# Kernel tuning notes

Hardware: AMD Instinct MI355X
Metric: run time of the kernel (lower is better)

Reference implementation:

```python
import jax, jax.numpy as jnp
import numpy as np

N_DRUG = 50000
N_DIS = 50000
D = 128      # input feature dim (lazily inferred by GCNConv(-1, h))
H = 128      # hidden_channels
OUT = 64     # out_channels
E = 800000   # edges per relation
L = 2        # num_layers
NUM_REL = 4  # [drug-drug, dis-dis, drug->dis, dis->drug]


def setup_inputs() -> dict:
    key = jax.random.key(0)
    ks = jax.random.split(key, 10)
    x_drug = jax.random.normal(ks[0], (N_DRUG, D), jnp.float32)
    x_dis = jax.random.normal(ks[1], (N_DIS, D), jnp.float32)
    ei_dd = jax.random.randint(ks[2], (2, E), 0, N_DRUG, dtype=jnp.int32)
    ei_ss = jax.random.randint(ks[3], (2, E), 0, N_DIS, dtype=jnp.int32)
    ei_ds = jax.random.randint(ks[4], (2, E), 0, N_DRUG, dtype=jnp.int32)  # row<N_DRUG, col<N_DIS (equal sizes)
    ei_sd = jax.random.randint(ks[5], (2, E), 0, N_DIS, dtype=jnp.int32)
    # per-layer, per-relation GCN weights (glorot-ish scale) and biases
    Ws = jax.random.normal(ks[6], (L, NUM_REL, D, H), jnp.float32) * (1.0 / np.sqrt(D))
    bs = jnp.zeros((L, NUM_REL, H), jnp.float32)
    lin_w = jax.random.normal(ks[7], (OUT, H), jnp.float32) * (1.0 / np.sqrt(H))
    lin_b = jnp.zeros((OUT,), jnp.float32)
    return {"x_drug": x_drug, "x_dis": x_dis, "ei_dd": ei_dd, "ei_ss": ei_ss,
            "ei_ds": ei_ds, "ei_sd": ei_sd, "Ws": Ws, "bs": bs,
            "lin_w": lin_w, "lin_b": lin_b}


def _gcn(x_src, ei, n_src, n_dst, W, b, self_loops):
    """GCNConv: symmetric degree-normalized gather -> scatter-add -> linear."""
    row, col = ei[0], ei[1]
    if self_loops:  # homogeneous relation: add self loops (n_src == n_dst)
        idx = jnp.arange(n_dst, dtype=row.dtype)
        row = jnp.concatenate([row, idx])
        col = jnp.concatenate([col, idx])
    ones = jnp.ones(row.shape[0], x_src.dtype)
    deg_s = jax.ops.segment_sum(ones, row, num_segments=n_src)
    deg_d = jax.ops.segment_sum(ones, col, num_segments=n_dst)
    dinv_s = jnp.where(deg_s > 0, jax.lax.rsqrt(jnp.maximum(deg_s, 1.0)), 0.0)
    dinv_d = jnp.where(deg_d > 0, jax.lax.rsqrt(jnp.maximum(deg_d, 1.0)), 0.0)
    norm = dinv_s[row] * dinv_d[col]                      # [E]
    h = x_src @ W                                         # [n_src, H]
    out = jax.ops.segment_sum(h[row] * norm[:, None], col, num_segments=n_dst)
    return out + b


def reference(x_drug, x_dis, ei_dd, ei_ss, ei_ds, ei_sd, Ws, bs, lin_w, lin_b):
    for l in range(L):
        drug_new = (_gcn(x_drug, ei_dd, N_DRUG, N_DRUG, Ws[l, 0], bs[l, 0], True)
                    + _gcn(x_dis, ei_sd, N_DIS, N_DRUG, Ws[l, 3], bs[l, 3], False))
        dis_new = (_gcn(x_dis, ei_ss, N_DIS, N_DIS, Ws[l, 1], bs[l, 1], True)
                   + _gcn(x_drug, ei_ds, N_DRUG, N_DIS, Ws[l, 2], bs[l, 2], False))
        x_drug = jax.nn.relu(drug_new)
        x_dis = jax.nn.relu(dis_new)
    return (x_drug @ lin_w.T + lin_b, x_dis @ lin_w.T + lin_b)
```

## Files before the change

### kernel.cpp

```cpp
#include <hip/hip_runtime.h>

#define NV   50000
#define FD   128
#define NE   800000
#define NOUT 64
#define NBIN 196
#define CH   2048
#define NBLK 391
#define SCAN_L (NBIN * NBLK)
#define SCHUNK 2048
#define NSCH ((SCAN_L + SCHUNK - 1) / SCHUNK)
#define CAP2 12288

typedef unsigned short bf16_t;
typedef unsigned short u16;
typedef unsigned char  u8;
typedef __attribute__((ext_vector_type(8))) short bf16x8;
typedef __attribute__((ext_vector_type(4))) float f32x4;

__device__ __forceinline__ bf16_t f2bf(float f) {
  unsigned u = __builtin_bit_cast(unsigned, f);
  return (bf16_t)((u + 0x7fffu + ((u >> 16) & 1u)) >> 16);
}
__device__ __forceinline__ float bflo(unsigned v) { return __builtin_bit_cast(float, v << 16); }
__device__ __forceinline__ float bfhi(unsigned v) { return __builtin_bit_cast(float, v & 0xffff0000u); }

struct Ptr4 { const int* p[4]; };


__global__ __launch_bounds__(256) void p0_hist(Ptr4 rows, Ptr4 cols,
                                               int* __restrict__ blockCnt) {
  const int r = blockIdx.y, blk = blockIdx.x, t = threadIdx.x;
  __shared__ int cd[NBIN], cs[NBIN];
  for (int i = t; i < NBIN; i += 256) { cd[i] = 0; cs[i] = 0; }
  __syncthreads();
  const int e0 = blk * CH;
  const int n = min(CH, NE - e0);
  const int* rw = rows.p[r] + e0;
  const int* cl = cols.p[r] + e0;
  for (int i = t; i < n; i += 256) {
    atomicAdd(&cd[cl[i] >> 8], 1);
    atomicAdd(&cs[rw[i] >> 8], 1);
  }
  __syncthreads();
  int* bd = blockCnt + (size_t)(r * 2 + 0) * SCAN_L;
  int* bs = blockCnt + (size_t)(r * 2 + 1) * SCAN_L;
  for (int i = t; i < NBIN; i += 256) {
    bd[i * NBLK + blk] = cd[i];
    bs[i * NBLK + blk] = cs[i];
  }
}

__global__ __launch_bounds__(256) void scan_pass1(const int* __restrict__ blockCnt,
                                                  int* __restrict__ chunkSum) {
  const int r2 = blockIdx.y, chunk = blockIdx.x, t = threadIdx.x;
  const int* a = blockCnt + (size_t)r2 * SCAN_L + chunk * SCHUNK;
  const int n = min(SCHUNK, SCAN_L - chunk * SCHUNK);
  int s = 0;
  for (int i = t; i < n; i += 256) s += a[i];
  __shared__ int sm[256];
  sm[t] = s;
  __syncthreads();
  #pragma unroll
  for (int off = 128; off > 0; off >>= 1) {
    if (t < off) sm[t] += sm[t + off];
    __syncthreads();
  }
  if (t == 0) chunkSum[r2 * NSCH + chunk] = sm[0];
}

__global__ __launch_bounds__(512) void scan_pass2(int* __restrict__ chunkSum,
                                                  int* __restrict__ bucketBase) {
  const int t = threadIdx.x;
  __shared__ int sm[8 * NSCH];
  if (t < 8 * NSCH) sm[t] = chunkSum[t];
  __syncthreads();
  if (t < 8) {
    int run = 0;
    for (int j = 0; j < NSCH; ++j) {
      int v = sm[t * NSCH + j];
      sm[t * NSCH + j] = run;
      run += v;
    }
    bucketBase[t * (NBIN + 1) + NBIN] = NE;
  }
  __syncthreads();
  if (t < 8 * NSCH) chunkSum[t] = sm[t];
}

__global__ __launch_bounds__(256) void scan_pass3(int* __restrict__ blockCnt,
                                                  const int* __restrict__ chunkSum,
                                                  int* __restrict__ bucketBase) {
  const int r2 = blockIdx.y, chunk = blockIdx.x, t = threadIdx.x;
  int* a = blockCnt + (size_t)r2 * SCAN_L + chunk * SCHUNK;
  const int gbase = chunk * SCHUNK;
  const int n = min(SCHUNK, SCAN_L - gbase);
  const int idx0 = t * 8;
  int v[8];
  int s = 0;
  #pragma unroll
  for (int j = 0; j < 8; ++j) {
    int id = idx0 + j;
    v[j] = (id < n) ? a[id] : 0;
    s += v[j];
  }
  __shared__ int sm[256];
  sm[t] = s;
  __syncthreads();
  for (int off = 1; off < 256; off <<= 1) {
    int x = (t >= off) ? sm[t - off] : 0;
    __syncthreads();
    sm[t] += x;
    __syncthreads();
  }
  int pre = ((t == 0) ? 0 : sm[t - 1]) + chunkSum[r2 * NSCH + chunk];
  #pragma unroll
  for (int j = 0; j < 8; ++j) {
    int id = idx0 + j;
    if (id < n) {
      int val = v[j];
      a[id] = pre;
      int g = gbase + id;
      if (g % NBLK == 0) bucketBase[r2 * (NBIN + 1) + g / NBLK] = pre;
      pre += val;
    }
  }
}

__global__ __launch_bounds__(256) void p1_scatter(Ptr4 rows, Ptr4 cols,
                                                  const int* __restrict__ blockCnt,
                                                  unsigned* __restrict__ pairD,
                                                  u8* __restrict__ srcb) {
  const int r = blockIdx.y, blk = blockIdx.x, t = threadIdx.x;
  const int e0 = blk * CH;
  const int n = min(CH, NE - e0);
  const int* rw = rows.p[r] + e0;
  const int* cl = cols.p[r] + e0;

  __shared__ int cnt[256], sc[256], lofs[256], cnt2[256], baseT[256];
  __shared__ unsigned pr[CH];
  __shared__ u8 binb[CH];
  __shared__ u8 pay8[CH];

  cnt[t] = 0; cnt2[t] = 0;
  __syncthreads();
  for (int i = t; i < n; i += 256) atomicAdd(&cnt[cl[i] >> 8], 1);
  __syncthreads();
  sc[t] = cnt[t];
  __syncthreads();
  for (int off = 1; off < 256; off <<= 1) {
    int v = (t >= off) ? sc[t - off] : 0;
    __syncthreads();
    sc[t] += v;
    __syncthreads();
  }
  lofs[t] = (t == 0) ? 0 : sc[t - 1];
  if (t < NBIN) baseT[t] = blockCnt[(size_t)(r * 2 + 0) * SCAN_L + t * NBLK + blk];
  __syncthreads();
  for (int i = t; i < n; i += 256) {
    int c = cl[i];
    int bin = c >> 8;
    int rank = atomicAdd(&cnt2[bin], 1);
    int p = lofs[bin] + rank;
    pr[p] = ((unsigned)(c & 255) << 16) | (unsigned)rw[i];
    binb[p] = (u8)bin;
  }
  __syncthreads();
  {
    unsigned* pd = pairD + (size_t)r * NE;
    for (int i = t; i < n; i += 256) {
      int bin = binb[i];
      pd[baseT[bin] + (i - lofs[bin])] = pr[i];
    }
  }
  __syncthreads();

  cnt[t] = 0; cnt2[t] = 0;
  __syncthreads();
  for (int i = t; i < n; i += 256) atomicAdd(&cnt[rw[i] >> 8], 1);
  __syncthreads();
  sc[t] = cnt[t];
  __syncthreads();
  for (int off = 1; off < 256; off <<= 1) {
    int v = (t >= off) ? sc[t - off] : 0;
    __syncthreads();
    sc[t] += v;
    __syncthreads();
  }
  lofs[t] = (t == 0) ? 0 : sc[t - 1];
  if (t < NBIN) baseT[t] = blockCnt[(size_t)(r * 2 + 1) * SCAN_L + t * NBLK + blk];
  __syncthreads();
  for (int i = t; i < n; i += 256) {
    int sv = rw[i];
    int bin = sv >> 8;
    int rank = atomicAdd(&cnt2[bin], 1);
    int p = lofs[bin] + rank;
    pay8[p] = (u8)(sv & 255);
    binb[p] = (u8)bin;
  }
  __syncthreads();
  {
    u8* sb = srcb + (size_t)r * NE;
    for (int i = t; i < n; i += 256) {
      int bin = binb[i];
      sb[baseT[bin] + (i - lofs[bin])] = pay8[i];
    }
  }
}

__global__ __launch_bounds__(256) void p2_csr(const unsigned* __restrict__ pairD,
                                              const int* __restrict__ bucketBase,
                                              u16* __restrict__ srcidx,
                                              int* __restrict__ rowptr,
                                              float* __restrict__ dinvD) {
  const int r = blockIdx.y, bin = blockIdx.x, t = threadIdx.x;
  const int* bb = bucketBase + (r * 2 + 0) * (NBIN + 1);
  const int base = bb[bin], next = bb[bin + 1];
  const int span = next - base;
  const unsigned* pd = pairD + (size_t)r * NE + base;

  __shared__ int cnt[256], sc[256], ex[256], cnt2[256];
  __shared__ u16 lsrc[CAP2];
  cnt[t] = 0; cnt2[t] = 0;
  __syncthreads();
  for (int i = t; i < span; i += 256) atomicAdd(&cnt[pd[i] >> 16], 1);
  __syncthreads();
  sc[t] = cnt[t];
  __syncthreads();
  for (int off = 1; off < 256; off <<= 1) {
    int v = (t >= off) ? sc[t - off] : 0;
    __syncthreads();
    sc[t] += v;
    __syncthreads();
  }
  ex[t] = (t == 0) ? 0 : sc[t - 1];
  __syncthreads();

  const int node = (bin << 8) + t;
  if (node < NV) {
    rowptr[r * (NV + 1) + node] = base + ex[t];
    float deg = (float)cnt[t];
    dinvD[r * NV + node] = (r < 2) ? rsqrtf(deg + 1.f)
                                   : (deg > 0.f ? rsqrtf(deg) : 0.f);
  }
  if (bin == NBIN - 1 && t == 0) rowptr[r * (NV + 1) + NV] = NE;

  u16* so = srcidx + (size_t)r * NE + base;
  if (span <= CAP2) {
    for (int i = t; i < span; i += 256) {
      unsigned v = pd[i];
      int dl = v >> 16;
      int rank = atomicAdd(&cnt2[dl], 1);
      lsrc[ex[dl] + rank] = (u16)(v & 0xFFFFu);
    }
    __syncthreads();
    for (int i = t; i < span; i += 256) so[i] = lsrc[i];
  } else {
    for (int i = t; i < span; i += 256) {
      unsigned v = pd[i];
      int dl = v >> 16;
      int rank = atomicAdd(&cnt2[dl], 1);
      so[ex[dl] + rank] = (u16)(v & 0xFFFFu);
    }
  }
}

__global__ __launch_bounds__(256) void p2_srcdeg(const u8* __restrict__ srcb,
                                                 const int* __restrict__ bucketBase,
                                                 float* __restrict__ dinvS) {
  const int r = blockIdx.y, bin = blockIdx.x, t = threadIdx.x;
  const int* bb = bucketBase + (r * 2 + 1) * (NBIN + 1);
  const int base = bb[bin], next = bb[bin + 1];
  const int span = next - base;
  const u8* sb = srcb + (size_t)r * NE + base;
  __shared__ int cnt[256];
  cnt[t] = 0;
  __syncthreads();
  for (int i = t; i < span; i += 256) atomicAdd(&cnt[sb[i]], 1);
  __syncthreads();
  int node = (bin << 8) + t;
  if (node < NV) {
    float deg = (float)cnt[t];
    dinvS[r * NV + node] = (r < 2) ? rsqrtf(deg + 1.f)
                                   : (deg > 0.f ? rsqrtf(deg) : 0.f);
  }
}


__global__ __launch_bounds__(256) void xcvt(const float* __restrict__ x,
                                            bf16_t* __restrict__ xb, int n4) {
  int i = blockIdx.x * 256 + threadIdx.x;
  if (i < n4) {
    float4 v = *(const float4*)(x + (size_t)i * 4);
    unsigned a = (unsigned)f2bf(v.x) | ((unsigned)f2bf(v.y) << 16);
    unsigned b = (unsigned)f2bf(v.z) | ((unsigned)f2bf(v.w) << 16);
    *(uint2*)(xb + (size_t)i * 4) = make_uint2(a, b);
  }
}

__global__ __launch_bounds__(256) void wprep(const float* __restrict__ Wsrc,
                                             bf16_t* __restrict__ Wt) {
  int idx = blockIdx.x * 256 + threadIdx.x;
  if (idx < 8 * 128 * 128) {
    int i = idx >> 14, n = (idx >> 7) & 127, k = idx & 127;
    Wt[idx] = f2bf(Wsrc[(size_t)i * 16384 + k * 128 + n]);
  }
}

__global__ __launch_bounds__(256) void gemm_mfma(
    const bf16_t* __restrict__ Xb0, const bf16_t* __restrict__ Wt0,
    const float* __restrict__ dS0, bf16_t* __restrict__ H0,
    const bf16_t* __restrict__ Xb1, const bf16_t* __restrict__ Wt1,
    const float* __restrict__ dS1, bf16_t* __restrict__ H1) {
  const bf16_t* Xb; const bf16_t* Wt; const float* dS; bf16_t* H;
  if (blockIdx.y == 0) { Xb = Xb0; Wt = Wt0; dS = dS0; H = H0; }
  else                 { Xb = Xb1; Wt = Wt1; dS = dS1; H = H1; }

  __shared__ bf16_t Xs[128][136];
  __shared__ bf16_t Wsh[128][136];
  __shared__ float sdS[128];
  const int t = threadIdx.x;
  const int row0 = blockIdx.x * 128;

  #pragma unroll
  for (int j = 0; j < 8; ++j) {
    int r = (t >> 4) + j * 16;
    int c = (t & 15) * 8;
    int gr = row0 + r;
    uint4 v = make_uint4(0u, 0u, 0u, 0u);
    if (gr < NV) v = *(const uint4*)(Xb + (size_t)gr * FD + c);
    *(uint4*)&Xs[r][c] = v;
    *(uint4*)&Wsh[r][c] = *(const uint4*)(Wt + (size_t)r * FD + c);
  }
  if (t < 128) {
    int g = row0 + t;
    sdS[t] = (g < NV) ? dS[g] : 0.f;
  }
  __syncthreads();

  const int wave = t >> 6, lane = t & 63;
  const int lr = lane & 15;
  const int lk = (lane >> 4) * 8;
  const int mb = wave * 32;

  f32x4 acc[2][8];
  #pragma unroll
  for (int m = 0; m < 2; ++m)
    #pragma unroll
    for (int n = 0; n < 8; ++n) acc[m][n] = (f32x4){0.f, 0.f, 0.f, 0.f};

  #pragma unroll
  for (int kc = 0; kc < 128; kc += 32) {
    bf16x8 a0 = *(const bf16x8*)&Xs[mb + lr][kc + lk];
    bf16x8 a1 = *(const bf16x8*)&Xs[mb + 16 + lr][kc + lk];
    bf16x8 b[8];
    #pragma unroll
    for (int n = 0; n < 8; ++n) b[n] = *(const bf16x8*)&Wsh[n * 16 + lr][kc + lk];
    #pragma unroll
    for (int n = 0; n < 8; ++n) {
      acc[0][n] = __builtin_amdgcn_mfma_f32_16x16x32_bf16(a0, b[n], acc[0][n], 0, 0, 0);
      acc[1][n] = __builtin_amdgcn_mfma_f32_16x16x32_bf16(a1, b[n], acc[1][n], 0, 0, 0);
    }
  }

  __syncthreads();
  const int rgrp = (lane >> 4) * 4;
  #pragma unroll
  for (int m = 0; m < 2; ++m)
    #pragma unroll
    for (int n = 0; n < 8; ++n)
      #pragma unroll
      for (int j = 0; j < 4; ++j) {
        int rr = mb + m * 16 + rgrp + j;
        Wsh[rr][n * 16 + lr] = f2bf(acc[m][n][j] * sdS[rr]);
      }
  __syncthreads();

  #pragma unroll
  for (int j = 0; j < 8; ++j) {
    int r = (t >> 4) + j * 16;
    int c = (t & 15) * 8;
    int gr = row0 + r;
    if (gr < NV) *(uint4*)(H + (size_t)gr * FD + c) = *(const uint4*)&Wsh[r][c];
  }
}

__device__ __forceinline__ void gather_acc(const bf16_t* __restrict__ h,
                                           const u16* __restrict__ src,
                                           int p0, int p1, int d,
                                           float& ax, float& ay) {
  int p = p0;
  for (; p + 4 <= p1; p += 4) {
    int s0 = src[p], s1 = src[p + 1], s2 = src[p + 2], s3 = src[p + 3];
    unsigned v0 = *(const unsigned*)(h + ((size_t)s0 << 7) + d);
    unsigned v1 = *(const unsigned*)(h + ((size_t)s1 << 7) + d);
    unsigned v2 = *(const unsigned*)(h + ((size_t)s2 << 7) + d);
    unsigned v3 = *(const unsigned*)(h + ((size_t)s3 << 7) + d);
    ax += bflo(v0); ay += bfhi(v0);
    ax += bflo(v1); ay += bfhi(v1);
    ax += bflo(v2); ay += bfhi(v2);
    ax += bflo(v3); ay += bfhi(v3);
  }
  for (; p < p1; ++p) {
    int s = src[p];
    unsigned v = *(const unsigned*)(h + ((size_t)s << 7) + d);
    ax += bflo(v); ay += bfhi(v);
  }
}

__global__ __launch_bounds__(256) void pull2(
    const bf16_t* __restrict__ hA, const int* __restrict__ rpA, const u16* __restrict__ srcA,
    const float* __restrict__ dDA,
    const bf16_t* __restrict__ hB, const int* __restrict__ rpB, const u16* __restrict__ srcB,
    const float* __restrict__ dDB,
    const float* __restrict__ bA, const float* __restrict__ bB,
    bf16_t* __restrict__ Y) {
  const int i = (blockIdx.x * 256 + threadIdx.x) >> 6;
  const int lane = threadIdx.x & 63;
  if (i >= NV) return;
  const int d = lane * 2;

  float ax, ay;
  {
    unsigned v = *(const unsigned*)(hA + ((size_t)i << 7) + d);
    ax = bflo(v); ay = bfhi(v);
  }
  gather_acc(hA, srcA, rpA[i], rpA[i + 1], d, ax, ay);
  float bx = 0.f, by = 0.f;
  gather_acc(hB, srcB, rpB[i], rpB[i + 1], d, bx, by);

  float wA = dDA[i], wB = dDB[i];
  float ox = fmaf(ax, wA, fmaf(bx, wB, bA[d] + bB[d]));
  float oy = fmaf(ay, wA, fmaf(by, wB, bA[d + 1] + bB[d + 1]));
  unsigned pk = (unsigned)f2bf(fmaxf(ox, 0.f)) | ((unsigned)f2bf(fmaxf(oy, 0.f)) << 16);
  *(unsigned*)(Y + (size_t)i * FD + d) = pk;
}

__global__ __launch_bounds__(256) void linear64(const bf16_t* __restrict__ Xb,
                                                const float* __restrict__ lw,
                                                const float* __restrict__ lb,
                                                float* __restrict__ Out) {
  __shared__ float Wt[128][68];
  __shared__ float Xs[64][132];
  const int tid = threadIdx.x;
  const int row0 = blockIdx.x * 64;

  for (int i = tid * 4; i < 64 * 128; i += 1024) {
    float4 v = *(const float4*)(lw + i);
    int o = i >> 7, h = i & 127;
    Wt[h + 0][o] = v.x; Wt[h + 1][o] = v.y; Wt[h + 2][o] = v.z; Wt[h + 3][o] = v.w;
  }
  for (int i = tid * 8; i < 64 * 128; i += 2048) {
    int rr = i >> 7, cc = i & 127;
    int gr = row0 + rr;
    uint4 v = make_uint4(0u, 0u, 0u, 0u);
    if (gr < NV) v = *(const uint4*)(Xb + (size_t)gr * FD + cc);
    unsigned* pv = (unsigned*)&v;
    #pragma unroll
    for (int q = 0; q < 4; ++q) {
      Xs[rr][cc + q * 2]     = bflo(pv[q]);
      Xs[rr][cc + q * 2 + 1] = bfhi(pv[q]);
    }
  }
  __syncthreads();

  const int tx = tid & 15, ty = tid >> 4;
  float acc[4][4];
  #pragma unroll
  for (int i = 0; i < 4; ++i)
    #pragma unroll
    for (int j = 0; j < 4; ++j) acc[i][j] = 0.f;

  for (int k = 0; k < 128; k += 4) {
    float4 xr[4], w[4];
    #pragma unroll
    for (int i = 0; i < 4; ++i) xr[i] = *(const float4*)&Xs[ty * 4 + i][k];
    #pragma unroll
    for (int j = 0; j < 4; ++j) w[j] = *(const float4*)&Wt[k + j][tx * 4];
    #pragma unroll
    for (int i = 0; i < 4; ++i) {
      const float* xv = (const float*)&xr[i];
      #pragma unroll
      for (int j = 0; j < 4; ++j) {
        float x = xv[j];
        acc[i][0] = fmaf(x, w[j].x, acc[i][0]);
        acc[i][1] = fmaf(x, w[j].y, acc[i][1]);
        acc[i][2] = fmaf(x, w[j].z, acc[i][2]);
        acc[i][3] = fmaf(x, w[j].w, acc[i][3]);
      }
    }
  }
  float4 bias = *(const float4*)(lb + tx * 4);
  #pragma unroll
  for (int i = 0; i < 4; ++i) {
    int gr = row0 + ty * 4 + i;
    if (gr < NV) {
      *(float4*)(Out + (size_t)gr * NOUT + tx * 4) =
          make_float4(acc[i][0] + bias.x, acc[i][1] + bias.y,
                      acc[i][2] + bias.z, acc[i][3] + bias.w);
    }
  }
}


extern "C" void kernel_launch(void* const* d_in, const int* in_sizes, int n_in,
                              void* d_out, int out_size, void* d_ws, size_t ws_size,
                              hipStream_t stream) {
  const float* x_drug = (const float*)d_in[0];
  const float* x_dis  = (const float*)d_in[1];
  const int* ei[4] = { (const int*)d_in[2], (const int*)d_in[3],
                       (const int*)d_in[4], (const int*)d_in[5] };
  const float* Ws = (const float*)d_in[6];
  const float* bs = (const float*)d_in[7];
  const float* lw = (const float*)d_in[8];
  const float* lb = (const float*)d_in[9];
  float* out = (float*)d_out;

  char* p = (char*)d_ws;
  auto take = [&](size_t bytes) -> void* {
    char* q = p;
    p += (bytes + 255) & ~(size_t)255;
    return (void*)q;
  };
  int* blockCnt   = (int*)take((size_t)8 * SCAN_L * sizeof(int));
  int* chunkSum   = (int*)take((size_t)8 * NSCH * sizeof(int));
  int* bucketBase = (int*)take((size_t)8 * (NBIN + 1) * sizeof(int));
  unsigned* pairD = (unsigned*)take((size_t)4 * NE * sizeof(unsigned));
  u8* srcb        = (u8*)take((size_t)4 * NE);
  u16* srcidx     = (u16*)take((size_t)4 * NE * sizeof(u16));
  int* rowptr     = (int*)take((size_t)4 * (NV + 1) * sizeof(int));
  float* dinvS    = (float*)take((size_t)4 * NV * sizeof(float));
  float* dinvD    = (float*)take((size_t)4 * NV * sizeof(float));
  bf16_t* hA  = (bf16_t*)take((size_t)NV * FD * sizeof(bf16_t));
  bf16_t* hB  = (bf16_t*)take((size_t)NV * FD * sizeof(bf16_t));
  bf16_t* xdb = (bf16_t*)take((size_t)NV * FD * sizeof(bf16_t));
  bf16_t* xsb = (bf16_t*)take((size_t)NV * FD * sizeof(bf16_t));
  bf16_t* Wtb = (bf16_t*)take((size_t)8 * FD * FD * sizeof(bf16_t));
  bf16_t* XD1 = (bf16_t*)take((size_t)NV * FD * sizeof(bf16_t));
  bf16_t* XS1 = (bf16_t*)take((size_t)NV * FD * sizeof(bf16_t));
  bf16_t* XD2 = (bf16_t*)take((size_t)NV * FD * sizeof(bf16_t));
  bf16_t* XS2 = (bf16_t*)take((size_t)NV * FD * sizeof(bf16_t));

  Ptr4 rows = {{ ei[0], ei[1], ei[2], ei[3] }};
  Ptr4 cols = {{ ei[0] + NE, ei[1] + NE, ei[2] + NE, ei[3] + NE }};

  p0_hist<<<dim3(NBLK, 4), 256, 0, stream>>>(rows, cols, blockCnt);
  scan_pass1<<<dim3(NSCH, 8), 256, 0, stream>>>(blockCnt, chunkSum);
  scan_pass2<<<1, 512, 0, stream>>>(chunkSum, bucketBase);
  scan_pass3<<<dim3(NSCH, 8), 256, 0, stream>>>(blockCnt, chunkSum, bucketBase);
  p1_scatter<<<dim3(NBLK, 4), 256, 0, stream>>>(rows, cols, blockCnt, pairD, srcb);
  p2_csr<<<dim3(NBIN, 4), 256, 0, stream>>>(pairD, bucketBase, srcidx, rowptr, dinvD);
  p2_srcdeg<<<dim3(NBIN, 4), 256, 0, stream>>>(srcb, bucketBase, dinvS);
  xcvt<<<(NV * FD / 4 + 255) / 256, 256, 0, stream>>>(x_drug, xdb, NV * FD / 4);
  xcvt<<<(NV * FD / 4 + 255) / 256, 256, 0, stream>>>(x_dis, xsb, NV * FD / 4);
  wprep<<<(8 * FD * FD + 255) / 256, 256, 0, stream>>>(Ws, Wtb);

  const dim3 GEMM_GRID((NV + 127) / 128, 2);
  const int PULL_GRID = NV * 64 / 256;
  const int LIN_GRID = (NV + 63) / 64;
  const bf16_t* xd = xdb;
  const bf16_t* xs = xsb;
  bf16_t* nextd[2] = {XD1, XD2};
  bf16_t* nexts[2] = {XS1, XS2};
  for (int l = 0; l < 2; ++l) {
    const bf16_t* W0 = Wtb + (size_t)(l * 4 + 0) * FD * FD;
    const bf16_t* W1 = Wtb + (size_t)(l * 4 + 1) * FD * FD;
    const bf16_t* W2 = Wtb + (size_t)(l * 4 + 2) * FD * FD;
    const bf16_t* W3 = Wtb + (size_t)(l * 4 + 3) * FD * FD;
    const float* b0 = bs + (l * 4 + 0) * FD;
    const float* b1 = bs + (l * 4 + 1) * FD;
    const float* b2 = bs + (l * 4 + 2) * FD;
    const float* b3 = bs + (l * 4 + 3) * FD;

    gemm_mfma<<<GEMM_GRID, 256, 0, stream>>>(xd, W0, dinvS + 0 * NV, hA,
                                             xs, W3, dinvS + 3 * NV, hB);
    pull2<<<PULL_GRID, 256, 0, stream>>>(
        hA, rowptr + 0 * (NV + 1), srcidx + (size_t)0 * NE, dinvD + 0 * NV,
        hB, rowptr + 3 * (NV + 1), srcidx + (size_t)3 * NE, dinvD + 3 * NV,
        b0, b3, nextd[l]);

    gemm_mfma<<<GEMM_GRID, 256, 0, stream>>>(xs, W1, dinvS + 1 * NV, hA,
                                             xd, W2, dinvS + 2 * NV, hB);
    pull2<<<PULL_GRID, 256, 0, stream>>>(
        hA, rowptr + 1 * (NV + 1), srcidx + (size_t)1 * NE, dinvD + 1 * NV,
        hB, rowptr + 2 * (NV + 1), srcidx + (size_t)2 * NE, dinvD + 2 * NV,
        b1, b2, nexts[l]);

    xd = nextd[l];
    xs = nexts[l];
  }

  linear64<<<LIN_GRID, 256, 0, stream>>>(xd, lw, lb, out);
  linear64<<<LIN_GRID, 256, 0, stream>>>(xs, lw, lb, out + (size_t)NV * NOUT);
}
```

Before: 485.4 us.

## Store GEMM output in feature-sliced layout and pull per slice

Measured after the change: 961.7 us. 1.98x slower.

```diff
diff --git a/kernel.cpp b/kernel.cpp
--- a/kernel.cpp
+++ b/kernel.cpp
@@ -11,6 +11,8 @@
 #define SCHUNK 2048
 #define NSCH ((SCAN_L + SCHUNK - 1) / SCHUNK)
 #define CAP2 12288
+#define NSLICE 8
+#define SDIM 16
 
 typedef unsigned short bf16_t;
 typedef unsigned short u16;
@@ -381,59 +383,69 @@
     int r = (t >> 4) + j * 16;
     int c = (t & 15) * 8;
     int gr = row0 + r;
-    if (gr < NV) *(uint4*)(H + (size_t)gr * FD + c) = *(const uint4*)&Wsh[r][c];
-  }
-}
-
-__device__ __forceinline__ void gather_acc(const bf16_t* __restrict__ h,
-                                           const u16* __restrict__ src,
-                                           int p0, int p1, int d,
-                                           float& ax, float& ay) {
-  int p = p0;
-  for (; p + 4 <= p1; p += 4) {
-    int s0 = src[p], s1 = src[p + 1], s2 = src[p + 2], s3 = src[p + 3];
-    unsigned v0 = *(const unsigned*)(h + ((size_t)s0 << 7) + d);
-    unsigned v1 = *(const unsigned*)(h + ((size_t)s1 << 7) + d);
-    unsigned v2 = *(const unsigned*)(h + ((size_t)s2 << 7) + d);
-    unsigned v3 = *(const unsigned*)(h + ((size_t)s3 << 7) + d);
-    ax += bflo(v0); ay += bfhi(v0);
-    ax += bflo(v1); ay += bfhi(v1);
-    ax += bflo(v2); ay += bfhi(v2);
-    ax += bflo(v3); ay += bfhi(v3);
-  }
-  for (; p < p1; ++p) {
-    int s = src[p];
-    unsigned v = *(const unsigned*)(h + ((size_t)s << 7) + d);
-    ax += bflo(v); ay += bfhi(v);
-  }
-}
-
-__global__ __launch_bounds__(256) void pull2(
+    if (gr < NV) {
+      int slice = c >> 4;
+      int off = c & 15;
+      *(uint4*)(H + ((size_t)slice * NV + gr) * SDIM + off) = *(const uint4*)&Wsh[r][c];
+    }
+  }
+}
+
+__global__ __launch_bounds__(256) void pull_sliced(
     const bf16_t* __restrict__ hA, const int* __restrict__ rpA, const u16* __restrict__ srcA,
     const float* __restrict__ dDA,
     const bf16_t* __restrict__ hB, const int* __restrict__ rpB, const u16* __restrict__ srcB,
     const float* __restrict__ dDB,
     const float* __restrict__ bA, const float* __restrict__ bB,
     bf16_t* __restrict__ Y) {
-  const int i = (blockIdx.x * 256 + threadIdx.x) >> 6;
-  const int lane = threadIdx.x & 63;
+  const int slice = blockIdx.x & 7;
+  const int grp   = blockIdx.x >> 3;
+  const int wave  = threadIdx.x >> 6;
+  const int lane  = threadIdx.x & 63;
+  const int i = grp * 4 + wave;
   if (i >= NV) return;
-  const int d = lane * 2;
-
-  float ax, ay;
+  const int es = lane >> 3, dp = lane & 7;
+
+  const bf16_t* hAs = hA + (size_t)slice * NV * SDIM;
+  const bf16_t* hBs = hB + (size_t)slice * NV * SDIM;
+
+  float ax = 0.f, ay = 0.f;
+  if (es == 0) {
+    unsigned v = *(const unsigned*)(hAs + ((size_t)i << 4) + dp * 2);
+    ax = bflo(v); ay = bfhi(v);
+  }
   {
-    unsigned v = *(const unsigned*)(hA + ((size_t)i << 7) + d);
-    ax = bflo(v); ay = bfhi(v);
-  }
-  gather_acc(hA, srcA, rpA[i], rpA[i + 1], d, ax, ay);
+    int p1 = rpA[i + 1];
+    for (int p = rpA[i] + es; p < p1; p += 8) {
+      int s = srcA[p];
+      unsigned v = *(const unsigned*)(hAs + ((size_t)s << 4) + dp * 2);
+      ax += bflo(v); ay += bfhi(v);
+    }
+  }
   float bx = 0.f, by = 0.f;
-  gather_acc(hB, srcB, rpB[i], rpB[i + 1], d, bx, by);
-
-  float wA = dDA[i], wB = dDB[i];
-  float ox = fmaf(ax, wA, fmaf(bx, wB, bA[d] + bB[d]));
-  float oy = fmaf(ay, wA, fmaf(by, wB, bA[d + 1] + bB[d + 1]));
-  unsigned pk = (unsigned)f2bf(fmaxf(ox, 0.f)) | ((unsigned)f2bf(fmaxf(oy, 0.f)) << 16);
-  *(unsigned*)(Y + (size_t)i * FD + d) = pk;
+  {
+    int p1 = rpB[i + 1];
+    for (int p = rpB[i] + es; p < p1; p += 8) {
+      int s = srcB[p];
+      unsigned v = *(const unsigned*)(hBs + ((size_t)s << 4) + dp * 2);
+      bx += bflo(v); by += bfhi(v);
+    }
+  }
+  #pragma unroll
+  for (int m = 8; m <= 32; m <<= 1) {
+    ax += __shfl_xor(ax, m, 64);
+    ay += __shfl_xor(ay, m, 64);
+    bx += __shfl_xor(bx, m, 64);
+    by += __shfl_xor(by, m, 64);
+  }
+  if (es == 0) {
+    float wA = dDA[i], wB = dDB[i];
+    int d = slice * SDIM + dp * 2;
+    float ox = fmaf(ax, wA, fmaf(bx, wB, bA[d] + bB[d]));
+    float oy = fmaf(ay, wA, fmaf(by, wB, bA[d + 1] + bB[d + 1]));
+    unsigned pk = (unsigned)f2bf(fmaxf(ox, 0.f)) | ((unsigned)f2bf(fmaxf(oy, 0.f)) << 16);
+    *(unsigned*)(Y + (size_t)i * FD + d) = pk;
+  }
 }
 
 __global__ __launch_bounds__(256) void linear64(const bf16_t* __restrict__ Xb,
@@ -556,7 +568,7 @@
   wprep<<<(8 * FD * FD + 255) / 256, 256, 0, stream>>>(Ws, Wtb);
 
   const dim3 GEMM_GRID((NV + 127) / 128, 2);
-  const int PULL_GRID = NV * 64 / 256;
+  const int PULL_GRID = ((NV + 3) / 4) * NSLICE;
   const int LIN_GRID = (NV + 63) / 64;
   const bf16_t* xd = xdb;
   const bf16_t* xs = xsb;
@@ -574,14 +586,14 @@
 
     gemm_mfma<<<GEMM_GRID, 256, 0, stream>>>(xd, W0, dinvS + 0 * NV, hA,
                                              xs, W3, dinvS + 3 * NV, hB);
-    pull2<<<PULL_GRID, 256, 0, stream>>>(
+    pull_sliced<<<PULL_GRID, 256, 0, stream>>>(
         hA, rowptr + 0 * (NV + 1), srcidx + (size_t)0 * NE, dinvD + 0 * NV,
         hB, rowptr + 3 * (NV + 1), srcidx + (size_t)3 * NE, dinvD + 3 * NV,
         b0, b3, nextd[l]);
 
     gemm_mfma<<<GEMM_GRID, 256, 0, stream>>>(xs, W1, dinvS + 1 * NV, hA,
                                              xd, W2, dinvS + 2 * NV, hB);
-    pull2<<<PULL_GRID, 256, 0, stream>>>(
+    pull_sliced<<<PULL_GRID, 256, 0, stream>>>(
         hA, rowptr + 1 * (NV + 1), srcidx + (size_t)1 * NE, dinvD + 1 * NV,
         hB, rowptr + 2 * (NV + 1), srcidx + (size_t)2 * NE, dinvD + 2 * NV,
         b1, b2, nexts[l]);
```

## Batch four relation GEMMs and both pull aggregations per layer into single launches

Applied to the files above, without the earlier changes.

Measured after the change: 422.5 us. -13.0%, faster.

```diff
diff --git a/kernel.cpp b/kernel.cpp
--- a/kernel.cpp
+++ b/kernel.cpp
@@ -13,7 +13,6 @@
 #define CAP2 12288
 
 typedef unsigned short bf16_t;
-typedef unsigned short u16;
 typedef unsigned char  u8;
 typedef __attribute__((ext_vector_type(8))) short bf16x8;
 typedef __attribute__((ext_vector_type(4))) float f32x4;
@@ -210,7 +209,7 @@
 
 __global__ __launch_bounds__(256) void p2_csr(const unsigned* __restrict__ pairD,
                                               const int* __restrict__ bucketBase,
-                                              u16* __restrict__ srcidx,
+                                              int* __restrict__ srcidx,
                                               int* __restrict__ rowptr,
                                               float* __restrict__ dinvD) {
   const int r = blockIdx.y, bin = blockIdx.x, t = threadIdx.x;
@@ -220,7 +219,7 @@
   const unsigned* pd = pairD + (size_t)r * NE + base;
 
   __shared__ int cnt[256], sc[256], ex[256], cnt2[256];
-  __shared__ u16 lsrc[CAP2];
+  __shared__ int lsrc[CAP2];
   cnt[t] = 0; cnt2[t] = 0;
   __syncthreads();
   for (int i = t; i < span; i += 256) atomicAdd(&cnt[pd[i] >> 16], 1);
@@ -245,13 +244,13 @@
   }
   if (bin == NBIN - 1 && t == 0) rowptr[r * (NV + 1) + NV] = NE;
 
-  u16* so = srcidx + (size_t)r * NE + base;
+  int* so = srcidx + (size_t)r * NE + base;
   if (span <= CAP2) {
     for (int i = t; i < span; i += 256) {
       unsigned v = pd[i];
       int dl = v >> 16;
       int rank = atomicAdd(&cnt2[dl], 1);
-      lsrc[ex[dl] + rank] = (u16)(v & 0xFFFFu);
+      lsrc[ex[dl] + rank] = (int)(v & 0xFFFFu);
     }
     __syncthreads();
     for (int i = t; i < span; i += 256) so[i] = lsrc[i];
@@ -260,7 +259,7 @@
       unsigned v = pd[i];
       int dl = v >> 16;
       int rank = atomicAdd(&cnt2[dl], 1);
-      so[ex[dl] + rank] = (u16)(v & 0xFFFFu);
+      so[ex[dl] + rank] = (int)(v & 0xFFFFu);
     }
   }
 }
@@ -307,14 +306,17 @@
   }
 }
 
-__global__ __launch_bounds__(256) void gemm_mfma(
-    const bf16_t* __restrict__ Xb0, const bf16_t* __restrict__ Wt0,
-    const float* __restrict__ dS0, bf16_t* __restrict__ H0,
-    const bf16_t* __restrict__ Xb1, const bf16_t* __restrict__ Wt1,
-    const float* __restrict__ dS1, bf16_t* __restrict__ H1) {
-  const bf16_t* Xb; const bf16_t* Wt; const float* dS; bf16_t* H;
-  if (blockIdx.y == 0) { Xb = Xb0; Wt = Wt0; dS = dS0; H = H0; }
-  else                 { Xb = Xb1; Wt = Wt1; dS = dS1; H = H1; }
+struct G4 {
+  const bf16_t* X[4];
+  const bf16_t* W[4];
+  const float*  dS[4];
+  bf16_t*       H[4];
+};
+
+__global__ __launch_bounds__(256) void gemm_quad(G4 g) {
+  const int q = blockIdx.y;
+  const bf16_t* Xb = g.X[q]; const bf16_t* Wt = g.W[q];
+  const float* dS = g.dS[q]; bf16_t* H = g.H[q];
 
   __shared__ bf16_t Xs[128][136];
   __shared__ bf16_t Wsh[128][136];
@@ -333,8 +335,8 @@
     *(uint4*)&Wsh[r][c] = *(const uint4*)(Wt + (size_t)r * FD + c);
   }
   if (t < 128) {
-    int g = row0 + t;
-    sdS[t] = (g < NV) ? dS[g] : 0.f;
+    int gidx = row0 + t;
+    sdS[t] = (gidx < NV) ? dS[gidx] : 0.f;
   }
   __syncthreads();
 
@@ -385,55 +387,74 @@
   }
 }
 
-__device__ __forceinline__ void gather_acc(const bf16_t* __restrict__ h,
-                                           const u16* __restrict__ src,
-                                           int p0, int p1, int d,
-                                           float& ax, float& ay) {
+__device__ __forceinline__ void gather8(const bf16_t* __restrict__ h,
+                                        const int* __restrict__ src,
+                                        int p0, int p1, int d,
+                                        float& ax, float& ay) {
   int p = p0;
-  for (; p + 4 <= p1; p += 4) {
-    int s0 = src[p], s1 = src[p + 1], s2 = src[p + 2], s3 = src[p + 3];
-    unsigned v0 = *(const unsigned*)(h + ((size_t)s0 << 7) + d);
-    unsigned v1 = *(const unsigned*)(h + ((size_t)s1 << 7) + d);
-    unsigned v2 = *(const unsigned*)(h + ((size_t)s2 << 7) + d);
-    unsigned v3 = *(const unsigned*)(h + ((size_t)s3 << 7) + d);
+  while (p + 8 <= p1) {
+    int s0 = src[p + 0], s1 = src[p + 1], s2 = src[p + 2], s3 = src[p + 3];
+    int s4 = src[p + 4], s5 = src[p + 5], s6 = src[p + 6], s7 = src[p + 7];
+    unsigned v0 = *(const unsigned*)(h + (s0 << 7) + d);
+    unsigned v1 = *(const unsigned*)(h + (s1 << 7) + d);
+    unsigned v2 = *(const unsigned*)(h + (s2 << 7) + d);
+    unsigned v3 = *(const unsigned*)(h + (s3 << 7) + d);
+    unsigned v4 = *(const unsigned*)(h + (s4 << 7) + d);
+    unsigned v5 = *(const unsigned*)(h + (s5 << 7) + d);
+    unsigned v6 = *(const unsigned*)(h + (s6 << 7) + d);
+    unsigned v7 = *(const unsigned*)(h + (s7 << 7) + d);
     ax += bflo(v0); ay += bfhi(v0);
     ax += bflo(v1); ay += bfhi(v1);
     ax += bflo(v2); ay += bfhi(v2);
     ax += bflo(v3); ay += bfhi(v3);
-  }
-  for (; p < p1; ++p) {
+    ax += bflo(v4); ay += bfhi(v4);
+    ax += bflo(v5); ay += bfhi(v5);
+    ax += bflo(v6); ay += bfhi(v6);
+    ax += bflo(v7); ay += bfhi(v7);
+    p += 8;
+  }
+  while (p + 2 <= p1) {
+    int s0 = src[p], s1 = src[p + 1];
+    unsigned v0 = *(const unsigned*)(h + (s0 << 7) + d);
+    unsigned v1 = *(const unsigned*)(h + (s1 << 7) + d);
+    ax += bflo(v0); ay += bfhi(v0);
+    ax += bflo(v1); ay += bfhi(v1);
+    p += 2;
+  }
+  if (p < p1) {
     int s = src[p];
-    unsigned v = *(const unsigned*)(h + ((size_t)s << 7) + d);
+    unsigned v = *(const unsigned*)(h + (s << 7) + d);
     ax += bflo(v); ay += bfhi(v);
   }
 }
 
-__global__ __launch_bounds__(256) void pull2(
-    const bf16_t* __restrict__ hA, const int* __restrict__ rpA, const u16* __restrict__ srcA,
-    const float* __restrict__ dDA,
-    const bf16_t* __restrict__ hB, const int* __restrict__ rpB, const u16* __restrict__ srcB,
-    const float* __restrict__ dDB,
-    const float* __restrict__ bA, const float* __restrict__ bB,
-    bf16_t* __restrict__ Y) {
-  const int i = (blockIdx.x * 256 + threadIdx.x) >> 6;
+struct PullSide {
+  const bf16_t* hA; const int* rpA; const int* srcA; const float* dDA;
+  const bf16_t* hB; const int* rpB; const int* srcB; const float* dDB;
+  const float* bA; const float* bB; bf16_t* Y;
+};
+
+__global__ __launch_bounds__(256) void pull_dual(PullSide s0, PullSide s1) {
+  const PullSide& a = blockIdx.y ? s1 : s0;
+  const int i = __builtin_amdgcn_readfirstlane(blockIdx.x * 4 + (threadIdx.x >> 6));
+  if (i >= NV) return;
   const int lane = threadIdx.x & 63;
-  if (i >= NV) return;
   const int d = lane * 2;
 
   float ax, ay;
   {
-    unsigned v = *(const unsigned*)(hA + ((size_t)i << 7) + d);
+    unsigned v = *(const unsigned*)(a.hA + (i << 7) + d);
     ax = bflo(v); ay = bfhi(v);
   }
-  gather_acc(hA, srcA, rpA[i], rpA[i + 1], d, ax, ay);
+  gather8(a.hA, a.srcA, a.rpA[i], a.rpA[i + 1], d, ax, ay);
   float bx = 0.f, by = 0.f;
-  gather_acc(hB, srcB, rpB[i], rpB[i + 1], d, bx, by);
-
-  float wA = dDA[i], wB = dDB[i];
-  float ox = fmaf(ax, wA, fmaf(bx, wB, bA[d] + bB[d]));
-  float oy = fmaf(ay, wA, fmaf(by, wB, bA[d + 1] + bB[d + 1]));
+  gather8(a.hB, a.srcB, a.rpB[i], a.rpB[i + 1], d, bx, by);
+
+  float wA = a.dDA[i], wB = a.dDB[i];
+  float ox = fmaf(ax, wA, fmaf(bx, wB, a.bA[d] + a.bB[d]));
+  float oy = fmaf(ay, wA, fmaf(by, wB, a.bA[d + 1] + a.bB[d + 1]));
   unsigned pk = (unsigned)f2bf(fmaxf(ox, 0.f)) | ((unsigned)f2bf(fmaxf(oy, 0.f)) << 16);
-  *(unsigned*)(Y + (size_t)i * FD + d) = pk;
+  *(unsigned*)(a.Y + (size_t)i * FD + d) = pk;
 }
 
 __global__ __launch_bounds__(256) void linear64(const bf16_t* __restrict__ Xb,
@@ -527,12 +548,14 @@
   int* bucketBase = (int*)take((size_t)8 * (NBIN + 1) * sizeof(int));
   unsigned* pairD = (unsigned*)take((size_t)4 * NE * sizeof(unsigned));
   u8* srcb        = (u8*)take((size_t)4 * NE);
-  u16* srcidx     = (u16*)take((size_t)4 * NE * sizeof(u16));
+  int* srcidx     = (int*)take((size_t)4 * NE * sizeof(int));
   int* rowptr     = (int*)take((size_t)4 * (NV + 1) * sizeof(int));
   float* dinvS    = (float*)take((size_t)4 * NV * sizeof(float));
   float* dinvD    = (float*)take((size_t)4 * NV * sizeof(float));
   bf16_t* hA  = (bf16_t*)take((size_t)NV * FD * sizeof(bf16_t));
   bf16_t* hB  = (bf16_t*)take((size_t)NV * FD * sizeof(bf16_t));
+  bf16_t* hC  = (bf16_t*)take((size_t)NV * FD * sizeof(bf16_t));
+  bf16_t* hD  = (bf16_t*)take((size_t)NV * FD * sizeof(bf16_t));
   bf16_t* xdb = (bf16_t*)take((size_t)NV * FD * sizeof(bf16_t));
   bf16_t* xsb = (bf16_t*)take((size_t)NV * FD * sizeof(bf16_t));
   bf16_t* Wtb = (bf16_t*)take((size_t)8 * FD * FD * sizeof(bf16_t));
@@ -555,8 +578,8 @@
   xcvt<<<(NV * FD / 4 + 255) / 256, 256, 0, stream>>>(x_dis, xsb, NV * FD / 4);
   wprep<<<(8 * FD * FD + 255) / 256, 256, 0, stream>>>(Ws, Wtb);
 
-  const dim3 GEMM_GRID((NV + 127) / 128, 2);
-  const int PULL_GRID = NV * 64 / 256;
+  const dim3 GEMM_GRID((NV + 127) / 128, 4);
+  const dim3 PULL_GRID((NV + 3) / 4, 2);
   const int LIN_GRID = (NV + 63) / 64;
   const bf16_t* xd = xdb;
   const bf16_t* xs = xsb;
@@ -572,19 +595,26 @@
     const float* b2 = bs + (l * 4 + 2) * FD;
     const float* b3 = bs + (l * 4 + 3) * FD;
 
-    gemm_mfma<<<GEMM_GRID, 256, 0, stream>>>(xd, W0, dinvS + 0 * NV, hA,
-                                             xs, W3, dinvS + 3 * NV, hB);
-    pull2<<<PULL_GRID, 256, 0, stream>>>(
-        hA, rowptr + 0 * (NV + 1), srcidx + (size_t)0 * NE, dinvD + 0 * NV,
-        hB, rowptr + 3 * (NV + 1), srcidx + (size_t)3 * NE, dinvD + 3 * NV,
-        b0, b3, nextd[l]);
-
-    gemm_mfma<<<GEMM_GRID, 256, 0, stream>>>(xs, W1, dinvS + 1 * NV, hA,
-                                             xd, W2, dinvS + 2 * NV, hB);
-    pull2<<<PULL_GRID, 256, 0, stream>>>(
-        hA, rowptr + 1 * (NV + 1), srcidx + (size_t)1 * NE, dinvD + 1 * NV,
-        hB, rowptr + 2 * (NV + 1), srcidx + (size_t)2 * NE, dinvD + 2 * NV,
-        b1, b2, nexts[l]);
+    G4 g;
+    g.X[0] = xd;  g.W[0] = W0; g.dS[0] = dinvS + 0 * NV; g.H[0] = hA;
+    g.X[1] = xs;  g.W[1] = W3; g.dS[1] = dinvS + 3 * NV; g.H[1] = hB;
+    g.X[2] = xs;  g.W[2] = W1; g.dS[2] = dinvS + 1 * NV; g.H[2] = hC;
+    g.X[3] = xd;  g.W[3] = W2; g.dS[3] = dinvS + 2 * NV; g.H[3] = hD;
+    gemm_quad<<<GEMM_GRID, 256, 0, stream>>>(g);
+
+    PullSide pd_;
+    pd_.hA = hA; pd_.rpA = rowptr + 0 * (NV + 1); pd_.srcA = srcidx + (size_t)0 * NE;
+    pd_.dDA = dinvD + 0 * NV;
+    pd_.hB = hB; pd_.rpB = rowptr + 3 * (NV + 1); pd_.srcB = srcidx + (size_t)3 * NE;
+    pd_.dDB = dinvD + 3 * NV;
+    pd_.bA = b0; pd_.bB = b3; pd_.Y = nextd[l];
+    PullSide ps_;
+    ps_.hA = hC; ps_.rpA = rowptr + 1 * (NV + 1); ps_.srcA = srcidx + (size_t)1 * NE;
+    ps_.dDA = dinvD + 1 * NV;
+    ps_.hB = hD; ps_.rpB = rowptr + 2 * (NV + 1); ps_.srcB = srcidx + (size_t)2 * NE;
+    ps_.dDB = dinvD + 2 * NV;
+    ps_.bA = b1; ps_.bB = b2; ps_.Y = nexts[l];
+    pull_dual<<<PULL_GRID, 256, 0, stream>>>(pd_, ps_);
 
     xd = nextd[l];
     xs = nexts[l];
```
